# Performance work log

Hardware: AMD Instinct MI355X
Metric: run time of the kernel (lower is better)

## Reference

```python
import jax, jax.numpy as jnp
import numpy as np

D_MODEL, JOINT_DIM, VOCAB = 512, 640, 1024
B, T, U = 4, 256, 64


def setup_inputs() -> dict:
    key = jax.random.key(0)
    ks = jax.random.split(key, 8)
    s_in = 1.0 / np.sqrt(D_MODEL)
    s_j = 1.0 / np.sqrt(JOINT_DIM)
    return {
        "enc": jax.random.normal(ks[0], (B, T, D_MODEL), jnp.float32),
        "pred": jax.random.normal(ks[1], (B, U, D_MODEL), jnp.float32),
        "enc_w": jax.random.uniform(ks[2], (JOINT_DIM, D_MODEL), jnp.float32, -s_in, s_in),
        "enc_b": jax.random.uniform(ks[3], (JOINT_DIM,), jnp.float32, -s_in, s_in),
        "pred_w": jax.random.uniform(ks[4], (JOINT_DIM, D_MODEL), jnp.float32, -s_in, s_in),
        "pred_b": jax.random.uniform(ks[5], (JOINT_DIM,), jnp.float32, -s_in, s_in),
        "out_w": jax.random.uniform(ks[6], (VOCAB, JOINT_DIM), jnp.float32, -s_j, s_j),
        "out_b": jax.random.uniform(ks[7], (VOCAB,), jnp.float32, -s_j, s_j),
    }


def reference(enc, pred, enc_w, enc_b, pred_w, pred_b, out_w, out_b):
    # project encoder (B,T,J) and predictor (B,U,J)
    e = jnp.einsum("btd,jd->btj", enc, enc_w) + enc_b
    p = jnp.einsum("bud,jd->buj", pred, pred_w) + pred_b
    # broadcast add over the (T,U) grid, tanh, then vocab projection
    z = jnp.tanh(e[:, :, None, :] + p[:, None, :, :])  # (B,T,U,J)
    logits = jnp.einsum("btuj,vj->btuv", z, out_w) + out_b  # (B,T,U,V)
    return logits
```

## Files before the change

### kernel.cpp

```cpp
#include <hip/hip_runtime.h>
#include <cstdint>
#include <cstddef>


typedef __attribute__((ext_vector_type(8))) __bf16 bf16x8;
typedef __attribute__((ext_vector_type(4))) float f32x4;

__device__ __forceinline__ int swz64(int row, int kElem) {
  return (row << 6) + (kElem ^ ((row & 7) << 3));
}
__device__ __forceinline__ int swz32(int row, int kElem) {
  return (row << 5) + ((kElem & 7) | (((kElem >> 3) ^ (row & 3)) << 3));
}

__device__ __forceinline__ float fast_tanh(float x) {
  float e = __builtin_amdgcn_exp2f(x * 2.88539008177793f);
  return 1.0f - 2.0f * __builtin_amdgcn_rcpf(e + 1.0f);
}

__device__ __forceinline__ void gload_lds16(const void* g, void* l) {
  __builtin_amdgcn_global_load_lds(
      (const __attribute__((address_space(1))) void*)g,
      (__attribute__((address_space(3))) void*)l, 16, 0, 0);
}

__device__ void proj_tile(const float* __restrict__ A, const float* __restrict__ W,
                          const float* __restrict__ bias, __bf16* __restrict__ C,
                          int mt, int nt, __bf16* As, __bf16* Bs)
{
  const int tid  = threadIdx.x;
  const int r = tid & 127, half = tid >> 7;
  const int lane = tid & 63, wv = tid >> 6;
  const int wm = wv >> 1, wn = wv & 1;

  const float* arow = A + (size_t)(mt * 128 + r) * 512 + half * 32;
  const float* wrow = W + (size_t)(nt * 128 + r) * 512 + half * 32;

  f32x4 acc[4][4] = {};

  for (int k0 = 0; k0 < 512; k0 += 64) {
#pragma unroll
    for (int s = 0; s < 4; ++s) {
      f32x4 a0 = *(const f32x4*)(arow + k0 + s * 8);
      f32x4 a1 = *(const f32x4*)(arow + k0 + s * 8 + 4);
      f32x4 w0 = *(const f32x4*)(wrow + k0 + s * 8);
      f32x4 w1 = *(const f32x4*)(wrow + k0 + s * 8 + 4);
      bf16x8 za, zw;
#pragma unroll
      for (int j = 0; j < 4; ++j) {
        za[j] = (__bf16)a0[j]; za[4 + j] = (__bf16)a1[j];
        zw[j] = (__bf16)w0[j]; zw[4 + j] = (__bf16)w1[j];
      }
      const int kk = half * 32 + s * 8;
      *(bf16x8*)&As[swz64(r, kk)] = za;
      *(bf16x8*)&Bs[swz64(r, kk)] = zw;
    }
    __syncthreads();
#pragma unroll
    for (int kk = 0; kk < 2; ++kk) {
      bf16x8 af[4], bfr[4];
#pragma unroll
      for (int i = 0; i < 4; ++i) {
        af[i]  = *(const bf16x8*)&As[swz64(wm * 64 + i * 16 + (lane & 15), kk * 32 + (lane >> 4) * 8)];
        bfr[i] = *(const bf16x8*)&Bs[swz64(wn * 64 + i * 16 + (lane & 15), kk * 32 + (lane >> 4) * 8)];
      }
#pragma unroll
      for (int mi = 0; mi < 4; ++mi)
#pragma unroll
        for (int ni = 0; ni < 4; ++ni)
          acc[mi][ni] = __builtin_amdgcn_mfma_f32_16x16x32_bf16(af[mi], bfr[ni], acc[mi][ni], 0, 0, 0);
    }
    __syncthreads();
  }

  const int rowbase = mt * 128 + wm * 64;
  const int colbase = nt * 128 + wn * 64;
#pragma unroll
  for (int ni = 0; ni < 4; ++ni) {
    const int col = colbase + ni * 16 + (lane & 15);
    const float bb = bias[col];
#pragma unroll
    for (int mi = 0; mi < 4; ++mi) {
      const int row = rowbase + mi * 16 + (lane >> 4) * 4;
#pragma unroll
      for (int rg = 0; rg < 4; ++rg)
        C[(size_t)(row + rg) * 640 + col] = (__bf16)(acc[mi][ni][rg] + bb);
    }
  }
}

__global__ __launch_bounds__(256) void prep_kernel(
    const float* __restrict__ enc,  const float* __restrict__ enc_w,  const float* __restrict__ enc_b,
    const float* __restrict__ pred, const float* __restrict__ pred_w, const float* __restrict__ pred_b,
    const float* __restrict__ out_w,
    __bf16* __restrict__ E, __bf16* __restrict__ P, __bf16* __restrict__ Wb, int zpath)
{
  __shared__ __align__(16) __bf16 As[128 * 64];
  __shared__ __align__(16) __bf16 Bs[128 * 64];
  const int bid = blockIdx.x;
  if (bid < 40) {
    proj_tile(enc, enc_w, enc_b, E, bid / 5, bid % 5, As, Bs);
  } else if (bid < 50) {
    proj_tile(pred, pred_w, pred_b, P, (bid - 40) / 5, (bid - 40) % 5, As, Bs);
  } else {
    const int gid = (bid - 50) * 256 + threadIdx.x;
    const int v  = gid / 80;
    const int j8 = gid % 80;
    f32x4 w0 = *(const f32x4*)(out_w + (size_t)v * 640 + j8 * 8);
    f32x4 w1 = *(const f32x4*)(out_w + (size_t)v * 640 + j8 * 8 + 4);
    bf16x8 z;
#pragma unroll
    for (int j = 0; j < 4; ++j) { z[j] = (__bf16)w0[j]; z[4 + j] = (__bf16)w1[j]; }
    if (zpath) {
      const int nt = v >> 8;
      const int half = (v >> 7) & 1;
      const int rr = v & 127;
      const int kt = j8 >> 2;
      const int kk = (j8 & 3) * 8;
      *(bf16x8*)(Wb + (((size_t)(nt * 20 + kt) * 2 + half) << 12) + swz32(rr, kk)) = z;
    } else {
      const int nb = v >> 7, rr = v & 127;
      const int kb = j8 >> 3, kk = (j8 & 7) * 8;
      *(bf16x8*)(Wb + ((size_t)(nb * 10 + kb) << 13) + swz64(rr, kk)) = z;
    }
  }
}

__global__ __launch_bounds__(256) void zprod_kernel(
    const __bf16* __restrict__ E, const __bf16* __restrict__ P,
    __bf16* __restrict__ Z)
{
  const int bid = blockIdx.x;
  const int mt = bid / 20, kt = bid % 20;
  __bf16* zdst = Z + ((size_t)bid << 12);

#pragma unroll
  for (int c = 0; c < 2; ++c) {
    const int o = c * 2048 + threadIdx.x * 8;
    const int r = o >> 5;
    const int cc = (o >> 3) & 3;
    const int k = kt * 32 + ((cc ^ (r & 3)) << 3);
    const int grow = mt * 128 + r;
    const __bf16* ep = E + (size_t)(grow >> 6) * 640 + k;
    const __bf16* pp = P + (size_t)(((grow >> 14) << 6) | (grow & 63)) * 640 + k;
    bf16x8 e8 = *(const bf16x8*)ep;
    bf16x8 p8 = *(const bf16x8*)pp;
    bf16x8 z;
#pragma unroll
    for (int j = 0; j < 8; ++j)
      z[j] = (__bf16)fast_tanh((float)e8[j] + (float)p8[j]);
    *(bf16x8*)&zdst[o] = z;
  }
}

__global__ __launch_bounds__(512, 4) void joiner_2ph(
    const __bf16* __restrict__ Z, const __bf16* __restrict__ Wb,
    const float* __restrict__ outb, float* __restrict__ out)
{
  __shared__ __align__(16) __bf16 As[2][4096];
  __shared__ __align__(16) __bf16 Bs[2][8192];
  const int wg = blockIdx.x;
  const int bid = (wg & 7) * 256 + (wg >> 3);
  const int mt = bid >> 2, nt = bid & 3;
  const int tid = threadIdx.x;
  const int lane = tid & 63, wv = tid >> 6;
  const int wm = wv >> 2, wn = wv & 3;
  const int q = lane & 15;
  const int chunk = (((lane >> 4) ^ (q & 3)) << 3);

  const __bf16* zsrc = Z  + (size_t)mt * 81920;
  const __bf16* wsrc = Wb + (size_t)nt * 163840;

  const int abase = (wm * 64 + q) * 32 + chunk;
  const int bbase = (wn * 64 + q) * 32 + chunk;

  f32x4 acc[4][4] = {};

  auto stage = [&](int k) {
    const int d = k & 1;
    const int wo = wv * 512;
    gload_lds16(zsrc + k * 4096 + wo + lane * 8, &As[d][wo]);
    gload_lds16(wsrc + k * 8192 + wo + lane * 8, &Bs[d][wo]);
    gload_lds16(wsrc + k * 8192 + 4096 + wo + lane * 8, &Bs[d][4096 + wo]);
  };

  stage(0);
  asm volatile("s_waitcnt vmcnt(0)" ::: "memory");
  __builtin_amdgcn_s_barrier();

#pragma unroll 2
  for (int k = 0; k < 20; ++k) {
    const int d = k & 1;
    if (k < 19) stage(k + 1);
    bf16x8 af[4], bfr[4];
#pragma unroll
    for (int mi = 0; mi < 4; ++mi)
      af[mi] = *(const bf16x8*)&As[d][abase + mi * 512];
#pragma unroll
    for (int ni = 0; ni < 4; ++ni)
      bfr[ni] = *(const bf16x8*)&Bs[d][bbase + ni * 512];
    __builtin_amdgcn_s_setprio(1);
#pragma unroll
    for (int mi = 0; mi < 4; ++mi)
#pragma unroll
      for (int ni = 0; ni < 4; ++ni)
        acc[mi][ni] = __builtin_amdgcn_mfma_f32_16x16x32_bf16(af[mi], bfr[ni], acc[mi][ni], 0, 0, 0);
    __builtin_amdgcn_s_setprio(0);
    if (k < 19) {
      asm volatile("s_waitcnt vmcnt(0)" ::: "memory");
      __builtin_amdgcn_s_barrier();
    }
  }

  const int rowbase = (mt << 7) + wm * 64;
  const int colbase = (nt << 8) + wn * 64;
#pragma unroll
  for (int ni = 0; ni < 4; ++ni) {
    const int col = colbase + ni * 16 + q;
    const float bb = outb[col];
#pragma unroll
    for (int mi = 0; mi < 4; ++mi) {
      const int row = rowbase + mi * 16 + (lane >> 4) * 4;
#pragma unroll
      for (int rg = 0; rg < 4; ++rg)
        out[(size_t)(row + rg) * 1024 + col] = acc[mi][ni][rg] + bb;
    }
  }
}

__global__ __launch_bounds__(512, 4) void joiner_fused(
    const __bf16* __restrict__ E, const __bf16* __restrict__ P,
    const __bf16* __restrict__ Wb, const float* __restrict__ outb,
    float* __restrict__ out)
{
  __shared__ __align__(16) __bf16 As[8192];
  __shared__ __align__(16) __bf16 Bs[2][16384];
  const int tid = threadIdx.x;
  const int nt = blockIdx.x & 3;
  const int mt = blockIdx.x >> 2;
  const int row0 = mt << 7;
  const int b  = row0 >> 14;
  const int t0 = (row0 >> 6) & 255;
  const int ar = tid & 127, h = tid >> 7;
  const int lane = tid & 63, wv = tid >> 6;
  const int wm = wv >> 2, wn = wv & 3;

  const __bf16* ep = E + (size_t)((b << 8) + t0 + (ar >> 6)) * 640 + h * 16;
  const __bf16* pp = P + (size_t)((b << 6) + (ar & 63)) * 640 + h * 16;

  f32x4 acc[4][4] = {};
  bf16x8 eA[2], pA[2];

  auto stageB2 = [&](int kt, __bf16* dst) {
#pragma unroll
    for (int c = 0; c < 4; ++c) {
      const int blk = nt * 2 + (c >> 1);
      const int inoff = (c & 1) * 4096 + wv * 512;
      gload_lds16(Wb + ((size_t)(blk * 10 + kt) << 13) + inoff + lane * 8,
                  dst + (c >> 1) * 8192 + inoff);
    }
  };
  auto loadEP = [&](int k0) {
#pragma unroll
    for (int c = 0; c < 2; ++c) {
      eA[c] = *(const bf16x8*)(ep + k0 + c * 8);
      pA[c] = *(const bf16x8*)(pp + k0 + c * 8);
    }
  };
  auto writeA = [&]() {
#pragma unroll
    for (int c = 0; c < 2; ++c) {
      bf16x8 z;
#pragma unroll
      for (int j = 0; j < 8; ++j)
        z[j] = (__bf16)fast_tanh((float)eA[c][j] + (float)pA[c][j]);
      *(bf16x8*)&As[swz64(ar, h * 16 + c * 8)] = z;
    }
  };
  auto compute = [&](const __bf16* Bsc) {
#pragma unroll
    for (int kk = 0; kk < 2; ++kk) {
      bf16x8 af[4], bfr[4];
#pragma unroll
      for (int i = 0; i < 4; ++i) {
        af[i]  = *(const bf16x8*)&As[swz64(wm * 64 + i * 16 + (lane & 15), kk * 32 + (lane >> 4) * 8)];
        bfr[i] = *(const bf16x8*)&Bsc[swz64(wn * 64 + i * 16 + (lane & 15), kk * 32 + (lane >> 4) * 8)];
      }
      asm volatile("s_waitcnt lgkmcnt(0)" ::: "memory");
      __builtin_amdgcn_sched_barrier(0);
      __builtin_amdgcn_s_setprio(1);
#pragma unroll
      for (int mi = 0; mi < 4; ++mi)
#pragma unroll
        for (int ni = 0; ni < 4; ++ni)
          acc[mi][ni] = __builtin_amdgcn_mfma_f32_16x16x32_bf16(af[mi], bfr[ni], acc[mi][ni], 0, 0, 0);
      __builtin_amdgcn_s_setprio(0);
    }
  };

  stageB2(0, Bs[0]);
  loadEP(0);
  writeA();
  asm volatile("s_waitcnt vmcnt(0) lgkmcnt(0)" ::: "memory");
  __builtin_amdgcn_s_barrier();

  for (int kt = 0; kt < 9; ++kt) {
    const int cur = kt & 1;
    stageB2(kt + 1, Bs[cur ^ 1]);
    loadEP((kt + 1) << 6);
    compute(Bs[cur]);
    __builtin_amdgcn_s_barrier();
    __builtin_amdgcn_sched_barrier(0);
    writeA();
    asm volatile("s_waitcnt lgkmcnt(0)" ::: "memory");
    __builtin_amdgcn_s_barrier();
  }
  compute(Bs[1]);

  const int rowbase = row0 + wm * 64;
  const int colbase = (nt << 8) + wn * 64;
#pragma unroll
  for (int ni = 0; ni < 4; ++ni) {
    const int col = colbase + ni * 16 + (lane & 15);
    const float bb = outb[col];
#pragma unroll
    for (int mi = 0; mi < 4; ++mi) {
      const int row = rowbase + mi * 16 + (lane >> 4) * 4;
#pragma unroll
      for (int rg = 0; rg < 4; ++rg)
        out[(size_t)(row + rg) * 1024 + col] = acc[mi][ni][rg] + bb;
    }
  }
}

extern "C" void kernel_launch(void* const* d_in, const int* in_sizes, int n_in,
                              void* d_out, int out_size, void* d_ws, size_t ws_size,
                              hipStream_t stream) {
  const float* enc    = (const float*)d_in[0];
  const float* pred   = (const float*)d_in[1];
  const float* enc_w  = (const float*)d_in[2];
  const float* enc_b  = (const float*)d_in[3];
  const float* pred_w = (const float*)d_in[4];
  const float* pred_b = (const float*)d_in[5];
  const float* out_w  = (const float*)d_in[6];
  const float* out_b  = (const float*)d_in[7];
  float* out = (float*)d_out;

  char* ws = (char*)d_ws;
  __bf16* E  = (__bf16*)(ws);
  __bf16* P  = (__bf16*)(ws + 1310720);
  __bf16* Wb = (__bf16*)(ws + 1638400);
  __bf16* Z  = (__bf16*)(ws + 2949120);

  const int zpath = (ws_size >= (size_t)86835200) ? 1 : 0;

  prep_kernel<<<dim3(370), dim3(256), 0, stream>>>(
      enc, enc_w, enc_b, pred, pred_w, pred_b, out_w, E, P, Wb, zpath);

  if (zpath) {
    zprod_kernel<<<dim3(10240), dim3(256), 0, stream>>>(E, P, Z);
    joiner_2ph<<<dim3(2048), dim3(512), 0, stream>>>(Z, Wb, out_b, out);
  } else {
    joiner_fused<<<dim3(2048), dim3(512), 0, stream>>>(E, P, Wb, out_b, out);
  }
}
```

Baseline: 163.0 us.

## Use three-slot LDS ring to prefetch two tiles ahead in joiner GEMM

Replaces the double-buffered joiner GEMM with a triple-buffered LDS ring. Each iteration issues loads two tiles ahead and waits only for the older batch (vmcnt(3)) rather than draining all outstanding loads. The intent is to hide global-to-LDS latency behind the MFMA work. LDS use rises to 72 KB per block, which could reduce how many blocks fit per CU. Barriers are also wrapped with compiler memory fences.

```diff
diff --git a/kernel.cpp b/kernel.cpp
--- a/kernel.cpp
+++ b/kernel.cpp
@@ -22,6 +22,12 @@
   __builtin_amdgcn_global_load_lds(
       (const __attribute__((address_space(1))) void*)g,
       (__attribute__((address_space(3))) void*)l, 16, 0, 0);
+}
+
+__device__ __forceinline__ void wg_barrier() {
+  asm volatile("" ::: "memory");
+  __builtin_amdgcn_s_barrier();
+  asm volatile("" ::: "memory");
 }
 
 __device__ void proj_tile(const float* __restrict__ A, const float* __restrict__ W,
@@ -153,12 +159,12 @@
   }
 }
 
-__global__ __launch_bounds__(512, 4) void joiner_2ph(
+__global__ __launch_bounds__(512, 4) void joiner_ring3(
     const __bf16* __restrict__ Z, const __bf16* __restrict__ Wb,
     const float* __restrict__ outb, float* __restrict__ out)
 {
-  __shared__ __align__(16) __bf16 As[2][4096];
-  __shared__ __align__(16) __bf16 Bs[2][8192];
+  __shared__ __align__(16) __bf16 As[3][4096];
+  __shared__ __align__(16) __bf16 Bs[3][8192];
   const int wg = blockIdx.x;
   const int bid = (wg & 7) * 256 + (wg >> 3);
   const int mt = bid >> 2, nt = bid & 3;
@@ -176,29 +182,27 @@
 
   f32x4 acc[4][4] = {};
 
-  auto stage = [&](int k) {
-    const int d = k & 1;
+  auto stage = [&](int k, int slot) {
     const int wo = wv * 512;
-    gload_lds16(zsrc + k * 4096 + wo + lane * 8, &As[d][wo]);
-    gload_lds16(wsrc + k * 8192 + wo + lane * 8, &Bs[d][wo]);
-    gload_lds16(wsrc + k * 8192 + 4096 + wo + lane * 8, &Bs[d][4096 + wo]);
-  };
-
-  stage(0);
-  asm volatile("s_waitcnt vmcnt(0)" ::: "memory");
-  __builtin_amdgcn_s_barrier();
-
-#pragma unroll 2
-  for (int k = 0; k < 20; ++k) {
-    const int d = k & 1;
-    if (k < 19) stage(k + 1);
+    gload_lds16(zsrc + k * 4096 + wo + lane * 8, &As[slot][wo]);
+    gload_lds16(wsrc + k * 8192 + wo + lane * 8, &Bs[slot][wo]);
+    gload_lds16(wsrc + k * 8192 + 4096 + wo + lane * 8, &Bs[slot][4096 + wo]);
+  };
+
+  auto iter = [&](int k, int slot, int stslot) {
     bf16x8 af[4], bfr[4];
 #pragma unroll
     for (int mi = 0; mi < 4; ++mi)
-      af[mi] = *(const bf16x8*)&As[d][abase + mi * 512];
+      af[mi] = *(const bf16x8*)&As[slot][abase + mi * 512];
 #pragma unroll
     for (int ni = 0; ni < 4; ++ni)
-      bfr[ni] = *(const bf16x8*)&Bs[d][bbase + ni * 512];
+      bfr[ni] = *(const bf16x8*)&Bs[slot][bbase + ni * 512];
+    if (k < 18) stage(k + 2, stslot);
+    if (k < 18)       asm volatile("s_waitcnt vmcnt(3)" ::: "memory");
+    else if (k == 18) asm volatile("s_waitcnt vmcnt(0)" ::: "memory");
+    wg_barrier();
+    asm volatile("s_waitcnt lgkmcnt(0)" ::: "memory");
+    __builtin_amdgcn_sched_barrier(0);
     __builtin_amdgcn_s_setprio(1);
 #pragma unroll
     for (int mi = 0; mi < 4; ++mi)
@@ -206,11 +210,22 @@
       for (int ni = 0; ni < 4; ++ni)
         acc[mi][ni] = __builtin_amdgcn_mfma_f32_16x16x32_bf16(af[mi], bfr[ni], acc[mi][ni], 0, 0, 0);
     __builtin_amdgcn_s_setprio(0);
-    if (k < 19) {
-      asm volatile("s_waitcnt vmcnt(0)" ::: "memory");
-      __builtin_amdgcn_s_barrier();
-    }
-  }
+    if (k < 19) wg_barrier();
+  };
+
+  stage(0, 0);
+  stage(1, 1);
+  asm volatile("s_waitcnt vmcnt(3)" ::: "memory");
+  wg_barrier();
+  wg_barrier();
+
+  for (int kb = 0; kb < 18; kb += 3) {
+    iter(kb,     0, 2);
+    iter(kb + 1, 1, 0);
+    iter(kb + 2, 2, 1);
+  }
+  iter(18, 0, 2);
+  iter(19, 1, 0);
 
   const int rowbase = (mt << 7) + wm * 64;
   const int colbase = (nt << 8) + wn * 64;
@@ -302,18 +317,18 @@
   loadEP(0);
   writeA();
   asm volatile("s_waitcnt vmcnt(0) lgkmcnt(0)" ::: "memory");
-  __builtin_amdgcn_s_barrier();
+  wg_barrier();
 
   for (int kt = 0; kt < 9; ++kt) {
     const int cur = kt & 1;
     stageB2(kt + 1, Bs[cur ^ 1]);
     loadEP((kt + 1) << 6);
     compute(Bs[cur]);
-    __builtin_amdgcn_s_barrier();
+    wg_barrier();
     __builtin_amdgcn_sched_barrier(0);
     writeA();
     asm volatile("s_waitcnt lgkmcnt(0)" ::: "memory");
-    __builtin_amdgcn_s_barrier();
+    wg_barrier();
   }
   compute(Bs[1]);
 
@@ -359,7 +374,7 @@
 
   if (zpath) {
     zprod_kernel<<<dim3(10240), dim3(256), 0, stream>>>(E, P, Z);
-    joiner_2ph<<<dim3(2048), dim3(512), 0, stream>>>(Z, Wb, out_b, out);
+    joiner_ring3<<<dim3(2048), dim3(512), 0, stream>>>(Z, Wb, out_b, out);
   } else {
     joiner_fused<<<dim3(2048), dim3(512), 0, stream>>>(E, P, Wb, out_b, out);
   }
```

Measured after the change: 172.8 us. 1.06x slower.
